# Kernel optimization log

Measured on AMD Instinct MI355X. Metric: run time of the kernel, lower is better.

The kernel has to match this reference:

```python
import jax, jax.numpy as jnp
import numpy as np

N = 100000   # num_nodes
E = 3200000  # num_edges (avg degree 32)
T = 16       # channels
L = 2        # n_layers


def setup_inputs() -> dict:
    key = jax.random.key(0)
    ks = jax.random.split(key, 6)
    x = jax.random.normal(ks[0], (T, N), dtype=jnp.float32)
    edge_index = jax.random.randint(ks[1], (2, E), 0, N)
    # per-layer scalar params (shared='all' -> shape [1,1] each), init U(-1,1)
    alpha1 = jax.random.uniform(ks[2], (L, 1, 1), minval=-1.0, maxval=1.0, dtype=jnp.float32)
    alpha2 = jax.random.uniform(ks[3], (L, 1, 1), minval=-1.0, maxval=1.0, dtype=jnp.float32)
    gamma = jax.random.uniform(ks[4], (L, 1, 1), minval=-1.0, maxval=1.0, dtype=jnp.float32)
    bias = jax.random.uniform(ks[5], (L, 1, 1), minval=-1.0, maxval=1.0, dtype=jnp.float32)
    return {"x": x, "edge_index": edge_index, "alpha1": alpha1,
            "alpha2": alpha2, "gamma": gamma, "bias": bias}


def reference(x, edge_index, alpha1, alpha2, gamma, bias):
    # DGMRF forward (transpose=False, with_bias=True): stack of L DGMRFLayerMultiChannel
    src, dst = edge_index[0], edge_index[1]
    # degrees = ptg.utils.degree(edge_index[0]) (out-degree of source nodes)
    deg = jax.ops.segment_sum(jnp.ones(E, dtype=x.dtype), src, num_segments=N)
    log_deg = jnp.log(deg)[None, :]          # [1, N]
    edge_log_deg = log_deg[0, dst][None, :]  # [1, E] = log_degrees[edge_index[1]] (non-transpose)
    for l in range(L):
        dp = jax.nn.sigmoid(gamma[l])        # degree_power, [1,1]
        sw = jnp.exp(alpha1[l])              # self_weight
        # NOTE: source's alpha2 property returns alpha1_param when shared != 'dynamics'
        nw = sw * jnp.tanh(alpha1[l])        # neighbor_weight
        weighted_repr = x * jnp.exp(dp * log_deg)        # [T, N]
        ew = jnp.exp((dp - 1.0) * edge_log_deg)          # [1, E] (base edge_weights are ones)
        msg = x[:, src] * ew                              # gather + weight: [T, E]
        agg = jnp.zeros_like(x).at[:, dst].add(msg)       # scatter-add aggregate
        x = sw * weighted_repr + nw * agg + bias[l]
    return x
```

## Files before the change

### kernel.cpp

```cpp
#include <hip/hip_runtime.h>


#define TCH 16
#define BBITS 8
#define BINW (1 << BBITS)
#define BLK 256
#define SPILL_CAP 65536

__global__ void k_hist(const int* __restrict__ src, const int* __restrict__ dst,
                       int* __restrict__ Hd, int* __restrict__ Hs,
                       int E, int NB, int CHUNK) {
    extern __shared__ int sm[];
    int* cd = sm; int* cs2 = sm + NB;
    for (int i = threadIdx.x; i < 2 * NB; i += blockDim.x) sm[i] = 0;
    __syncthreads();
    int beg = blockIdx.x * CHUNK;
    int end = beg + CHUNK; if (end > E) end = E;
    for (int i = beg + threadIdx.x; i < end; i += blockDim.x) {
        atomicAdd(&cd[dst[i] >> BBITS], 1);
        atomicAdd(&cs2[src[i] >> BBITS], 1);
    }
    __syncthreads();
    int* hd = Hd + (size_t)blockIdx.x * NB;
    int* hs = Hs + (size_t)blockIdx.x * NB;
    for (int b = threadIdx.x; b < NB; b += blockDim.x) { hd[b] = cd[b]; hs[b] = cs2[b]; }
}

__global__ void k_scanb(const int* __restrict__ H, int* __restrict__ off,
                        int* __restrict__ cnt, int NB, int NBLK) {
    __shared__ int ss[BLK];
    int bin = blockIdx.x;
    int t = threadIdx.x;
    int v[4];
    int sum = 0;
#pragma unroll
    for (int j = 0; j < 4; ++j) {
        int b = t * 4 + j;
        v[j] = (b < NBLK) ? H[(size_t)b * NB + bin] : 0;
        sum += v[j];
    }
    ss[t] = sum;
    __syncthreads();
    for (int o = 1; o < BLK; o <<= 1) {
        int u = (t >= o) ? ss[t - o] : 0;
        __syncthreads();
        ss[t] += u;
        __syncthreads();
    }
    int base = ss[t] - sum;
#pragma unroll
    for (int j = 0; j < 4; ++j) {
        int b = t * 4 + j;
        if (b < NBLK) off[(size_t)b * NB + bin] = base;
        base += v[j];
    }
    if (t == BLK - 1) cnt[bin] = ss[BLK - 1];
}

__global__ __launch_bounds__(BLK) void k_place(
        const int* __restrict__ src, const int* __restrict__ dst,
        const int* __restrict__ offd, const int* __restrict__ offs,
        int* __restrict__ dpairs, unsigned char* __restrict__ srcb,
        int* __restrict__ spill_cnt, int* __restrict__ spill_d,
        int* __restrict__ spill_s,
        int E, int NB, int CHUNK, int CAPB) {
    __shared__ int ss[BLK];
    extern __shared__ int sm[];
    int* cur = sm;
    int* gdl = sm + NB;
    int* pay = sm + 2 * NB;
    int* ga  = sm + 2 * NB + CHUNK;

    int t = threadIdx.x;
    int beg = blockIdx.x * CHUNK;
    int end = beg + CHUNK; if (end > E) end = E;
    int m = end - beg;

    for (int i = t; i < NB; i += BLK) cur[i] = 0;
    __syncthreads();
    for (int i = beg + t; i < end; i += BLK)
        atomicAdd(&cur[dst[i] >> BBITS], 1);
    __syncthreads();
    int c0 = (2 * t     < NB) ? cur[2 * t]     : 0;
    int c1 = (2 * t + 1 < NB) ? cur[2 * t + 1] : 0;
    ss[t] = c0 + c1;
    __syncthreads();
    for (int o = 1; o < BLK; o <<= 1) {
        int v = (t >= o) ? ss[t - o] : 0;
        __syncthreads();
        ss[t] += v;
        __syncthreads();
    }
    int excl = ss[t] - (c0 + c1);
    __syncthreads();
    if (2 * t < NB) {
        int od = offd[(size_t)blockIdx.x * NB + 2 * t];
        cur[2 * t] = excl;
        gdl[2 * t] = 2 * t * CAPB + od - excl;
    }
    if (2 * t + 1 < NB) {
        int od = offd[(size_t)blockIdx.x * NB + 2 * t + 1];
        cur[2 * t + 1] = excl + c0;
        gdl[2 * t + 1] = (2 * t + 1) * CAPB + od - (excl + c0);
    }
    __syncthreads();
    for (int i = beg + t; i < end; i += BLK) {
        int d = dst[i], s = src[i];
        int bd = d >> BBITS;
        int ls = atomicAdd(&cur[bd], 1);
        int g  = gdl[bd] + ls;
        if (g < (bd + 1) * CAPB) {
            pay[ls] = ((d & (BINW - 1)) << 24) | s;
            ga[ls] = g;
        } else {
            ga[ls] = -1;
            int p = atomicAdd(&spill_cnt[0], 1);
            if (p < SPILL_CAP) { spill_d[2 * p] = d; spill_d[2 * p + 1] = s; }
        }
    }
    __syncthreads();
    for (int i = t; i < m; i += BLK) {
        int g = ga[i];
        if (g >= 0) dpairs[g] = pay[i];
    }
    __syncthreads();

    unsigned char* payb = (unsigned char*)pay;
    for (int i = t; i < NB; i += BLK) cur[i] = 0;
    __syncthreads();
    for (int i = beg + t; i < end; i += BLK)
        atomicAdd(&cur[src[i] >> BBITS], 1);
    __syncthreads();
    c0 = (2 * t     < NB) ? cur[2 * t]     : 0;
    c1 = (2 * t + 1 < NB) ? cur[2 * t + 1] : 0;
    ss[t] = c0 + c1;
    __syncthreads();
    for (int o = 1; o < BLK; o <<= 1) {
        int v = (t >= o) ? ss[t - o] : 0;
        __syncthreads();
        ss[t] += v;
        __syncthreads();
    }
    excl = ss[t] - (c0 + c1);
    __syncthreads();
    if (2 * t < NB) {
        int os_ = offs[(size_t)blockIdx.x * NB + 2 * t];
        cur[2 * t] = excl;
        gdl[2 * t] = 2 * t * CAPB + os_ - excl;
    }
    if (2 * t + 1 < NB) {
        int os_ = offs[(size_t)blockIdx.x * NB + 2 * t + 1];
        cur[2 * t + 1] = excl + c0;
        gdl[2 * t + 1] = (2 * t + 1) * CAPB + os_ - (excl + c0);
    }
    __syncthreads();
    for (int i = beg + t; i < end; i += BLK) {
        int s = src[i];
        int bs = s >> BBITS;
        int ls = atomicAdd(&cur[bs], 1);
        int g  = gdl[bs] + ls;
        if (g < (bs + 1) * CAPB) {
            payb[ls] = (unsigned char)(s & (BINW - 1));
            ga[ls] = g;
        } else {
            ga[ls] = -1;
            int p = atomicAdd(&spill_cnt[1], 1);
            if (p < SPILL_CAP) spill_s[p] = s;
        }
    }
    __syncthreads();
    for (int i = t; i < m; i += BLK) {
        int g = ga[i];
        if (g >= 0) srcb[g] = payb[i];
    }
}

__global__ void k_binsort(const int* __restrict__ dpairs, const int* __restrict__ cntd,
                          const unsigned char* __restrict__ srcb, const int* __restrict__ cnts,
                          int* __restrict__ adj, int* __restrict__ rptr,
                          int* __restrict__ rcnt, int* __restrict__ deg,
                          int N, int CAPB) {
    __shared__ int h[BINW];
    __shared__ int o[BINW];
    __shared__ int rk[BINW];
    __shared__ int hd[BINW];
    int bin = blockIdx.x;
    int t = threadIdx.x;
    h[t] = 0; rk[t] = 0; hd[t] = 0;
    __syncthreads();
    int m = cntd[bin]; if (m > CAPB) m = CAPB;
    const int* pp = dpairs + (size_t)bin * CAPB;
    for (int i = t; i < m; i += blockDim.x)
        atomicAdd(&h[((unsigned)pp[i]) >> 24], 1);
    int ms = cnts[bin]; if (ms > CAPB) ms = CAPB;
    const unsigned char* sp = srcb + (size_t)bin * CAPB;
    for (int i = t; i < ms; i += blockDim.x)
        atomicAdd(&hd[sp[i]], 1);
    __syncthreads();
    o[t] = h[t];
    __syncthreads();
    for (int s = 1; s < BINW; s <<= 1) {
        int v = 0;
        if (t >= s) v = o[t - s];
        __syncthreads();
        if (t >= s) o[t] += v;
        __syncthreads();
    }
    int binbase = bin * CAPB;
    {
        int excl = o[t] - h[t];
        o[t] = excl;
        int n = (bin << BBITS) + t;
        if (n < N) { rptr[n] = binbase + excl; rcnt[n] = h[t]; deg[n] = hd[t]; }
    }
    __syncthreads();
    for (int i = t; i < m; i += blockDim.x) {
        int w = pp[i];
        int dl = ((unsigned)w) >> 24;
        int s  = w & 0xFFFFFF;
        int r = atomicAdd(&rk[dl], 1);
        adj[binbase + o[dl] + r] = s;
    }
}

__global__ void k_deg_spill(const int* __restrict__ spill_cnt, const int* __restrict__ spill_s,
                            int* __restrict__ deg) {
    int total = spill_cnt[1]; if (total > SPILL_CAP) total = SPILL_CAP;
    int stride = gridDim.x * blockDim.x;
    for (int i = blockIdx.x * blockDim.x + threadIdx.x; i < total; i += stride)
        atomicAdd(&deg[spill_s[i]], 1);
}

__global__ void k_tin(const float* __restrict__ x, float* __restrict__ xt, int N) {
    int n = blockIdx.x * blockDim.x + threadIdx.x;
    if (n >= N) return;
    float v[TCH];
#pragma unroll
    for (int t = 0; t < TCH; ++t) v[t] = x[(size_t)t * N + n];
    float4* o = reinterpret_cast<float4*>(xt + (size_t)n * TCH);
    o[0] = make_float4(v[0],  v[1],  v[2],  v[3]);
    o[1] = make_float4(v[4],  v[5],  v[6],  v[7]);
    o[2] = make_float4(v[8],  v[9],  v[10], v[11]);
    o[3] = make_float4(v[12], v[13], v[14], v[15]);
}

__global__ void k_layer(const float* __restrict__ xin, float* __restrict__ xout,
                        const int* __restrict__ rptr, const int* __restrict__ rcnt,
                        const int* __restrict__ adj, const int* __restrict__ deg,
                        const float* __restrict__ a1p, const float* __restrict__ gp,
                        const float* __restrict__ bp, int l, int N,
                        int last, float* __restrict__ out) {
    int tt = blockIdx.x * blockDim.x + threadIdx.x;
    int n = tt >> 2;
    int q = tt & 3;
    if (n >= N) return;
    float a1 = a1p[l], g = gp[l], bi = bp[l];
    float dp = 1.0f / (1.0f + expf(-g));
    float sw = expf(a1);
    float nw = sw * tanhf(a1);

    int b = rptr[n], m = rcnt[n];
    const int* row = adj + b;
    float4 acc0 = make_float4(0.f, 0.f, 0.f, 0.f);
    float4 acc1 = make_float4(0.f, 0.f, 0.f, 0.f);
    float4 acc2 = make_float4(0.f, 0.f, 0.f, 0.f);
    float4 acc3 = make_float4(0.f, 0.f, 0.f, 0.f);
    int i = 0;
    for (; i + 7 < m; i += 8) {
        int s0 = row[i],     s1 = row[i + 1], s2 = row[i + 2], s3 = row[i + 3];
        int s4 = row[i + 4], s5 = row[i + 5], s6 = row[i + 6], s7 = row[i + 7];
        float4 x0 = reinterpret_cast<const float4*>(xin + (size_t)s0 * TCH)[q];
        float4 x1 = reinterpret_cast<const float4*>(xin + (size_t)s1 * TCH)[q];
        float4 x2 = reinterpret_cast<const float4*>(xin + (size_t)s2 * TCH)[q];
        float4 x3 = reinterpret_cast<const float4*>(xin + (size_t)s3 * TCH)[q];
        float4 x4 = reinterpret_cast<const float4*>(xin + (size_t)s4 * TCH)[q];
        float4 x5 = reinterpret_cast<const float4*>(xin + (size_t)s5 * TCH)[q];
        float4 x6 = reinterpret_cast<const float4*>(xin + (size_t)s6 * TCH)[q];
        float4 x7 = reinterpret_cast<const float4*>(xin + (size_t)s7 * TCH)[q];
        acc0.x += x0.x; acc0.y += x0.y; acc0.z += x0.z; acc0.w += x0.w;
        acc1.x += x1.x; acc1.y += x1.y; acc1.z += x1.z; acc1.w += x1.w;
        acc2.x += x2.x; acc2.y += x2.y; acc2.z += x2.z; acc2.w += x2.w;
        acc3.x += x3.x; acc3.y += x3.y; acc3.z += x3.z; acc3.w += x3.w;
        acc0.x += x4.x; acc0.y += x4.y; acc0.z += x4.z; acc0.w += x4.w;
        acc1.x += x5.x; acc1.y += x5.y; acc1.z += x5.z; acc1.w += x5.w;
        acc2.x += x6.x; acc2.y += x6.y; acc2.z += x6.z; acc2.w += x6.w;
        acc3.x += x7.x; acc3.y += x7.y; acc3.z += x7.z; acc3.w += x7.w;
    }
    for (; i < m; ++i) {
        int s0 = row[i];
        float4 x0 = reinterpret_cast<const float4*>(xin + (size_t)s0 * TCH)[q];
        acc0.x += x0.x; acc0.y += x0.y; acc0.z += x0.z; acc0.w += x0.w;
    }
    acc0.x += acc1.x + acc2.x + acc3.x;
    acc0.y += acc1.y + acc2.y + acc3.y;
    acc0.z += acc1.z + acc2.z + acc3.z;
    acc0.w += acc1.w + acc2.w + acc3.w;

    float ldg = logf((float)deg[n]);
    float cs = sw * expf(dp * ldg);
    float cn = nw * expf((dp - 1.0f) * ldg);

    float4 xq = reinterpret_cast<const float4*>(xin + (size_t)n * TCH)[q];
    float4 r;
    r.x = cs * xq.x + cn * acc0.x + bi;
    r.y = cs * xq.y + cn * acc0.y + bi;
    r.z = cs * xq.z + cn * acc0.z + bi;
    r.w = cs * xq.w + cn * acc0.w + bi;

    if (last) {
        int t0 = q * 4;
        out[(size_t)(t0 + 0) * N + n] = r.x;
        out[(size_t)(t0 + 1) * N + n] = r.y;
        out[(size_t)(t0 + 2) * N + n] = r.z;
        out[(size_t)(t0 + 3) * N + n] = r.w;
    } else {
        reinterpret_cast<float4*>(xout + (size_t)n * TCH)[q] = r;
    }
}

__global__ void k_spill(const int* __restrict__ spill_cnt, const int* __restrict__ spill_d,
                        const float* __restrict__ xin, float* __restrict__ xout,
                        const int* __restrict__ deg,
                        const float* __restrict__ a1p, const float* __restrict__ gp,
                        int l, int N, int last, float* __restrict__ out) {
    int total = spill_cnt[0]; if (total > SPILL_CAP) total = SPILL_CAP;
    int stride = gridDim.x * blockDim.x;
    float a1 = a1p[l], g = gp[l];
    float dp = 1.0f / (1.0f + expf(-g));
    float nw = expf(a1) * tanhf(a1);
    for (int p = blockIdx.x * blockDim.x + threadIdx.x; p < total; p += stride) {
        int d = spill_d[2 * p], s = spill_d[2 * p + 1];
        float cn = nw * expf((dp - 1.0f) * logf((float)deg[d]));
#pragma unroll
        for (int t = 0; t < TCH; ++t) {
            float v = cn * xin[(size_t)s * TCH + t];
            if (last) atomicAdd(&out[(size_t)t * N + d], v);
            else      atomicAdd(&xout[(size_t)d * TCH + t], v);
        }
    }
}

extern "C" void kernel_launch(void* const* d_in, const int* in_sizes, int n_in,
                              void* d_out, int out_size, void* d_ws, size_t ws_size,
                              hipStream_t stream) {
    const float* x      = (const float*)d_in[0];
    const int*   ei     = (const int*)d_in[1];
    const float* alpha1 = (const float*)d_in[2];
    const float* gamma  = (const float*)d_in[4];
    const float* bias   = (const float*)d_in[5];
    float* out = (float*)d_out;

    const int N = in_sizes[0] / TCH;
    const int E = in_sizes[1] / 2;
    const int L = in_sizes[2];
    const int* src = ei;
    const int* dst = ei + E;

    const int NB = (N + BINW - 1) >> BBITS;
    int CHUNK = 4096;
    int NBLK = (E + CHUNK - 1) / CHUNK;
    while (NBLK > 4 * BLK) { CHUNK *= 2; NBLK = (E + CHUNK - 1) / CHUNK; }

    auto align = [](size_t v) { return (v + 255) & ~(size_t)255; };
    char* ws = (char*)d_ws;
    size_t off = 0;
    int* deg     = (int*)(ws + off); off += align((size_t)N * 4);
    int* rptr    = (int*)(ws + off); off += align((size_t)N * 4);
    int* rcnt    = (int*)(ws + off); off += align((size_t)N * 4);
    int* cntd    = (int*)(ws + off); off += align((size_t)NB * 4);
    int* cnts    = (int*)(ws + off); off += align((size_t)NB * 4);
    int* Hd      = (int*)(ws + off); off += align((size_t)NBLK * NB * 4);
    int* Hs      = (int*)(ws + off); off += align((size_t)NBLK * NB * 4);
    int* offd    = (int*)(ws + off); off += align((size_t)NBLK * NB * 4);
    int* offs    = (int*)(ws + off); off += align((size_t)NBLK * NB * 4);
    int* spill_c = (int*)(ws + off); off += 256;
    int* spill_d = (int*)(ws + off); off += align((size_t)SPILL_CAP * 8);
    int* spill_s = (int*)(ws + off); off += align((size_t)SPILL_CAP * 4);
    float* xt0   = (float*)(ws + off); off += align((size_t)N * TCH * 4);
    float* xt1   = (float*)(ws + off); off += align((size_t)N * TCH * 4);
    long long avg = ((long long)E * BINW + N - 1) / N;
    int CAPB = (int)(avg + avg / 16 + 64);
    size_t rem = (ws_size > off) ? (ws_size - off) : 0;
    size_t cap_fit = rem / ((size_t)NB * 9 + 8);
    if ((size_t)CAPB > cap_fit) CAPB = (int)cap_fit;
    if (CAPB < 1) CAPB = 1;
    int* dpairs  = (int*)(ws + off); off += align((size_t)NB * CAPB * 4);
    int* adj     = (int*)(ws + off); off += align((size_t)NB * CAPB * 4);
    unsigned char* srcb = (unsigned char*)(ws + off);

    dim3 b(BLK), gN((N + BLK - 1) / BLK);
    dim3 gN4(((size_t)N * 4 + BLK - 1) / BLK);

    size_t place_lds = ((size_t)2 * NB + 2 * CHUNK) * 4;

    hipMemsetAsync(spill_c, 0, 256, stream);
    k_hist   <<<dim3(NBLK), b, 2 * NB * 4, stream>>>(src, dst, Hd, Hs, E, NB, CHUNK);
    k_scanb  <<<dim3(NB),   b, 0,          stream>>>(Hd, offd, cntd, NB, NBLK);
    k_scanb  <<<dim3(NB),   b, 0,          stream>>>(Hs, offs, cnts, NB, NBLK);
    k_place  <<<dim3(NBLK), b, place_lds,  stream>>>(src, dst, offd, offs, dpairs, srcb,
                                                     spill_c, spill_d, spill_s,
                                                     E, NB, CHUNK, CAPB);
    k_binsort<<<dim3(NB),   b, 0,          stream>>>(dpairs, cntd, srcb, cnts,
                                                     adj, rptr, rcnt, deg, N, CAPB);
    k_deg_spill<<<dim3(16), b, 0,          stream>>>(spill_c, spill_s, deg);
    k_tin    <<<gN,         b, 0,          stream>>>(x, xt0, N);

    float* xin = xt0;
    float* xo  = xt1;
    for (int l = 0; l < L; ++l) {
        int last = (l == L - 1) ? 1 : 0;
        k_layer<<<gN4, b, 0, stream>>>(xin, xo, rptr, rcnt, adj, deg,
                                       alpha1, gamma, bias, l, N, last, out);
        k_spill<<<dim3(16), b, 0, stream>>>(spill_c, spill_d, xin, xo, deg,
                                            alpha1, gamma, l, N, last, out);
        float* tmp = xin; xin = xo; xo = tmp;
    }
}
```

Before: 198.4 us.

## Replace histogram+scan bucketing with atomic global cursors and LDS-staged bin sort

Removes the k_hist and two k_scanb passes. Each k_place block now reserves its per-bin output range with global atomicAdd on cursor arrays, which also serve as the bin counts. k_binsort stages the sorted adjacency in LDS and writes it out coalesced. The layer kernel uses nontemporal loads for the adjacency and row pointers. The trade-off is nondeterministic edge order within bins, a cap on CAPB so the LDS buffer fits, and possible atomic contention on the cursors.

```diff
diff --git a/kernel.cpp b/kernel.cpp
--- a/kernel.cpp
+++ b/kernel.cpp
@@ -7,59 +7,9 @@
 #define BLK 256
 #define SPILL_CAP 65536
 
-__global__ void k_hist(const int* __restrict__ src, const int* __restrict__ dst,
-                       int* __restrict__ Hd, int* __restrict__ Hs,
-                       int E, int NB, int CHUNK) {
-    extern __shared__ int sm[];
-    int* cd = sm; int* cs2 = sm + NB;
-    for (int i = threadIdx.x; i < 2 * NB; i += blockDim.x) sm[i] = 0;
-    __syncthreads();
-    int beg = blockIdx.x * CHUNK;
-    int end = beg + CHUNK; if (end > E) end = E;
-    for (int i = beg + threadIdx.x; i < end; i += blockDim.x) {
-        atomicAdd(&cd[dst[i] >> BBITS], 1);
-        atomicAdd(&cs2[src[i] >> BBITS], 1);
-    }
-    __syncthreads();
-    int* hd = Hd + (size_t)blockIdx.x * NB;
-    int* hs = Hs + (size_t)blockIdx.x * NB;
-    for (int b = threadIdx.x; b < NB; b += blockDim.x) { hd[b] = cd[b]; hs[b] = cs2[b]; }
-}
-
-__global__ void k_scanb(const int* __restrict__ H, int* __restrict__ off,
-                        int* __restrict__ cnt, int NB, int NBLK) {
-    __shared__ int ss[BLK];
-    int bin = blockIdx.x;
-    int t = threadIdx.x;
-    int v[4];
-    int sum = 0;
-#pragma unroll
-    for (int j = 0; j < 4; ++j) {
-        int b = t * 4 + j;
-        v[j] = (b < NBLK) ? H[(size_t)b * NB + bin] : 0;
-        sum += v[j];
-    }
-    ss[t] = sum;
-    __syncthreads();
-    for (int o = 1; o < BLK; o <<= 1) {
-        int u = (t >= o) ? ss[t - o] : 0;
-        __syncthreads();
-        ss[t] += u;
-        __syncthreads();
-    }
-    int base = ss[t] - sum;
-#pragma unroll
-    for (int j = 0; j < 4; ++j) {
-        int b = t * 4 + j;
-        if (b < NBLK) off[(size_t)b * NB + bin] = base;
-        base += v[j];
-    }
-    if (t == BLK - 1) cnt[bin] = ss[BLK - 1];
-}
-
 __global__ __launch_bounds__(BLK) void k_place(
         const int* __restrict__ src, const int* __restrict__ dst,
-        const int* __restrict__ offd, const int* __restrict__ offs,
+        int* __restrict__ gcur_d, int* __restrict__ gcur_s,
         int* __restrict__ dpairs, unsigned char* __restrict__ srcb,
         int* __restrict__ spill_cnt, int* __restrict__ spill_d,
         int* __restrict__ spill_s,
@@ -92,16 +42,15 @@
         __syncthreads();
     }
     int excl = ss[t] - (c0 + c1);
-    __syncthreads();
     if (2 * t < NB) {
-        int od = offd[(size_t)blockIdx.x * NB + 2 * t];
+        int gb = (c0 > 0) ? atomicAdd(&gcur_d[2 * t], c0) : 0;
         cur[2 * t] = excl;
-        gdl[2 * t] = 2 * t * CAPB + od - excl;
+        gdl[2 * t] = 2 * t * CAPB + gb - excl;
     }
     if (2 * t + 1 < NB) {
-        int od = offd[(size_t)blockIdx.x * NB + 2 * t + 1];
+        int gb = (c1 > 0) ? atomicAdd(&gcur_d[2 * t + 1], c1) : 0;
         cur[2 * t + 1] = excl + c0;
-        gdl[2 * t + 1] = (2 * t + 1) * CAPB + od - (excl + c0);
+        gdl[2 * t + 1] = (2 * t + 1) * CAPB + gb - (excl + c0);
     }
     __syncthreads();
     for (int i = beg + t; i < end; i += BLK) {
@@ -142,16 +91,15 @@
         __syncthreads();
     }
     excl = ss[t] - (c0 + c1);
-    __syncthreads();
     if (2 * t < NB) {
-        int os_ = offs[(size_t)blockIdx.x * NB + 2 * t];
+        int gb = (c0 > 0) ? atomicAdd(&gcur_s[2 * t], c0) : 0;
         cur[2 * t] = excl;
-        gdl[2 * t] = 2 * t * CAPB + os_ - excl;
+        gdl[2 * t] = 2 * t * CAPB + gb - excl;
     }
     if (2 * t + 1 < NB) {
-        int os_ = offs[(size_t)blockIdx.x * NB + 2 * t + 1];
+        int gb = (c1 > 0) ? atomicAdd(&gcur_s[2 * t + 1], c1) : 0;
         cur[2 * t + 1] = excl + c0;
-        gdl[2 * t + 1] = (2 * t + 1) * CAPB + os_ - (excl + c0);
+        gdl[2 * t + 1] = (2 * t + 1) * CAPB + gb - (excl + c0);
     }
     __syncthreads();
     for (int i = beg + t; i < end; i += BLK) {
@@ -175,26 +123,28 @@
     }
 }
 
-__global__ void k_binsort(const int* __restrict__ dpairs, const int* __restrict__ cntd,
-                          const unsigned char* __restrict__ srcb, const int* __restrict__ cnts,
-                          int* __restrict__ adj, int* __restrict__ rptr,
-                          int* __restrict__ rcnt, int* __restrict__ deg,
-                          int N, int CAPB) {
+__global__ __launch_bounds__(BLK) void k_binsort(
+        const int* __restrict__ dpairs, const int* __restrict__ cntd,
+        const unsigned char* __restrict__ srcb, const int* __restrict__ cnts,
+        int* __restrict__ adj, int* __restrict__ rptr,
+        int* __restrict__ rcnt, int* __restrict__ deg,
+        int N, int CAPB) {
     __shared__ int h[BINW];
     __shared__ int o[BINW];
     __shared__ int rk[BINW];
     __shared__ int hd[BINW];
+    extern __shared__ int lbuf[];
     int bin = blockIdx.x;
     int t = threadIdx.x;
     h[t] = 0; rk[t] = 0; hd[t] = 0;
     __syncthreads();
     int m = cntd[bin]; if (m > CAPB) m = CAPB;
     const int* pp = dpairs + (size_t)bin * CAPB;
-    for (int i = t; i < m; i += blockDim.x)
+    for (int i = t; i < m; i += BLK)
         atomicAdd(&h[((unsigned)pp[i]) >> 24], 1);
     int ms = cnts[bin]; if (ms > CAPB) ms = CAPB;
     const unsigned char* sp = srcb + (size_t)bin * CAPB;
-    for (int i = t; i < ms; i += blockDim.x)
+    for (int i = t; i < ms; i += BLK)
         atomicAdd(&hd[sp[i]], 1);
     __syncthreads();
     o[t] = h[t];
@@ -214,13 +164,16 @@
         if (n < N) { rptr[n] = binbase + excl; rcnt[n] = h[t]; deg[n] = hd[t]; }
     }
     __syncthreads();
-    for (int i = t; i < m; i += blockDim.x) {
+    for (int i = t; i < m; i += BLK) {
         int w = pp[i];
         int dl = ((unsigned)w) >> 24;
         int s  = w & 0xFFFFFF;
         int r = atomicAdd(&rk[dl], 1);
-        adj[binbase + o[dl] + r] = s;
-    }
+        lbuf[o[dl] + r] = s;
+    }
+    __syncthreads();
+    for (int i = t; i < m; i += BLK)
+        adj[binbase + i] = lbuf[i];
 }
 
 __global__ void k_deg_spill(const int* __restrict__ spill_cnt, const int* __restrict__ spill_s,
@@ -259,7 +212,8 @@
     float sw = expf(a1);
     float nw = sw * tanhf(a1);
 
-    int b = rptr[n], m = rcnt[n];
+    int b = __builtin_nontemporal_load(rptr + n);
+    int m = __builtin_nontemporal_load(rcnt + n);
     const int* row = adj + b;
     float4 acc0 = make_float4(0.f, 0.f, 0.f, 0.f);
     float4 acc1 = make_float4(0.f, 0.f, 0.f, 0.f);
@@ -267,8 +221,14 @@
     float4 acc3 = make_float4(0.f, 0.f, 0.f, 0.f);
     int i = 0;
     for (; i + 7 < m; i += 8) {
-        int s0 = row[i],     s1 = row[i + 1], s2 = row[i + 2], s3 = row[i + 3];
-        int s4 = row[i + 4], s5 = row[i + 5], s6 = row[i + 6], s7 = row[i + 7];
+        int s0 = __builtin_nontemporal_load(row + i);
+        int s1 = __builtin_nontemporal_load(row + i + 1);
+        int s2 = __builtin_nontemporal_load(row + i + 2);
+        int s3 = __builtin_nontemporal_load(row + i + 3);
+        int s4 = __builtin_nontemporal_load(row + i + 4);
+        int s5 = __builtin_nontemporal_load(row + i + 5);
+        int s6 = __builtin_nontemporal_load(row + i + 6);
+        int s7 = __builtin_nontemporal_load(row + i + 7);
         float4 x0 = reinterpret_cast<const float4*>(xin + (size_t)s0 * TCH)[q];
         float4 x1 = reinterpret_cast<const float4*>(xin + (size_t)s1 * TCH)[q];
         float4 x2 = reinterpret_cast<const float4*>(xin + (size_t)s2 * TCH)[q];
@@ -287,7 +247,7 @@
         acc3.x += x7.x; acc3.y += x7.y; acc3.z += x7.z; acc3.w += x7.w;
     }
     for (; i < m; ++i) {
-        int s0 = row[i];
+        int s0 = __builtin_nontemporal_load(row + i);
         float4 x0 = reinterpret_cast<const float4*>(xin + (size_t)s0 * TCH)[q];
         acc0.x += x0.x; acc0.y += x0.y; acc0.z += x0.z; acc0.w += x0.w;
     }
@@ -357,9 +317,8 @@
     const int* dst = ei + E;
 
     const int NB = (N + BINW - 1) >> BBITS;
-    int CHUNK = 4096;
-    int NBLK = (E + CHUNK - 1) / CHUNK;
-    while (NBLK > 4 * BLK) { CHUNK *= 2; NBLK = (E + CHUNK - 1) / CHUNK; }
+    const int CHUNK = 4096;
+    const int NBLK = (E + CHUNK - 1) / CHUNK;
 
     auto align = [](size_t v) { return (v + 255) & ~(size_t)255; };
     char* ws = (char*)d_ws;
@@ -367,13 +326,11 @@
     int* deg     = (int*)(ws + off); off += align((size_t)N * 4);
     int* rptr    = (int*)(ws + off); off += align((size_t)N * 4);
     int* rcnt    = (int*)(ws + off); off += align((size_t)N * 4);
-    int* cntd    = (int*)(ws + off); off += align((size_t)NB * 4);
-    int* cnts    = (int*)(ws + off); off += align((size_t)NB * 4);
-    int* Hd      = (int*)(ws + off); off += align((size_t)NBLK * NB * 4);
-    int* Hs      = (int*)(ws + off); off += align((size_t)NBLK * NB * 4);
-    int* offd    = (int*)(ws + off); off += align((size_t)NBLK * NB * 4);
-    int* offs    = (int*)(ws + off); off += align((size_t)NBLK * NB * 4);
+    size_t zbeg = off;
+    int* gcur_d  = (int*)(ws + off); off += align((size_t)NB * 4);
+    int* gcur_s  = (int*)(ws + off); off += align((size_t)NB * 4);
     int* spill_c = (int*)(ws + off); off += 256;
+    size_t zlen = off - zbeg;
     int* spill_d = (int*)(ws + off); off += align((size_t)SPILL_CAP * 8);
     int* spill_s = (int*)(ws + off); off += align((size_t)SPILL_CAP * 4);
     float* xt0   = (float*)(ws + off); off += align((size_t)N * TCH * 4);
@@ -384,6 +341,7 @@
     size_t cap_fit = rem / ((size_t)NB * 9 + 8);
     if ((size_t)CAPB > cap_fit) CAPB = (int)cap_fit;
     if (CAPB < 1) CAPB = 1;
+    if (CAPB > 30000) CAPB = 30000;
     int* dpairs  = (int*)(ws + off); off += align((size_t)NB * CAPB * 4);
     int* adj     = (int*)(ws + off); off += align((size_t)NB * CAPB * 4);
     unsigned char* srcb = (unsigned char*)(ws + off);
@@ -392,18 +350,17 @@
     dim3 gN4(((size_t)N * 4 + BLK - 1) / BLK);
 
     size_t place_lds = ((size_t)2 * NB + 2 * CHUNK) * 4;
-
-    hipMemsetAsync(spill_c, 0, 256, stream);
-    k_hist   <<<dim3(NBLK), b, 2 * NB * 4, stream>>>(src, dst, Hd, Hs, E, NB, CHUNK);
-    k_scanb  <<<dim3(NB),   b, 0,          stream>>>(Hd, offd, cntd, NB, NBLK);
-    k_scanb  <<<dim3(NB),   b, 0,          stream>>>(Hs, offs, cnts, NB, NBLK);
-    k_place  <<<dim3(NBLK), b, place_lds,  stream>>>(src, dst, offd, offs, dpairs, srcb,
-                                                     spill_c, spill_d, spill_s,
-                                                     E, NB, CHUNK, CAPB);
-    k_binsort<<<dim3(NB),   b, 0,          stream>>>(dpairs, cntd, srcb, cnts,
-                                                     adj, rptr, rcnt, deg, N, CAPB);
-    k_deg_spill<<<dim3(16), b, 0,          stream>>>(spill_c, spill_s, deg);
-    k_tin    <<<gN,         b, 0,          stream>>>(x, xt0, N);
+    size_t sort_lds  = (size_t)CAPB * 4;
+
+    hipMemsetAsync((void*)gcur_d, 0, zlen, stream);
+    k_place  <<<dim3(NBLK), b, place_lds, stream>>>(src, dst, gcur_d, gcur_s,
+                                                    dpairs, srcb,
+                                                    spill_c, spill_d, spill_s,
+                                                    E, NB, CHUNK, CAPB);
+    k_binsort<<<dim3(NB),   b, sort_lds,  stream>>>(dpairs, gcur_d, srcb, gcur_s,
+                                                    adj, rptr, rcnt, deg, N, CAPB);
+    k_deg_spill<<<dim3(16), b, 0,         stream>>>(spill_c, spill_s, deg);
+    k_tin    <<<gN,         b, 0,         stream>>>(x, xt0, N);
 
     float* xin = xt0;
     float* xo  = xt1;
```

New measurement: 221.5 us. +11.6%, slower.
